# Kernel tuning notes

Hardware: AMD Instinct MI355X
Metric: run time of the kernel (lower is better)

Reference implementation:

```python
import jax, jax.numpy as jnp
import numpy as np
import math

EMBED_DIM = 768
NUM_HEADS = 12


def setup_inputs() -> dict:
    key = jax.random.key(0)
    ks = jax.random.split(key, 5)
    R, C, B, E = 128, 256, 1, EMBED_DIM
    s = 1.0 / math.sqrt(E)
    x = jax.random.normal(ks[0], (R, C, B, E), dtype=jnp.float32)
    wq = jax.random.normal(ks[1], (E, E), dtype=jnp.float32) * s
    wk = jax.random.normal(ks[2], (E, E), dtype=jnp.float32) * s
    wv = jax.random.normal(ks[3], (E, E), dtype=jnp.float32) * s
    wo = jax.random.normal(ks[4], (E, E), dtype=jnp.float32) * s
    z = jnp.zeros((E,), dtype=jnp.float32)
    return {"x": x, "wq": wq, "bq": z, "wk": wk, "bk": z,
            "wv": wv, "bv": z, "wo": wo, "bo": z}


def reference(x, wq, bq, wk, bk, wv, bv, wo, bo):
    R, C, B, E = x.shape
    H = NUM_HEADS
    D = E // H
    shape = (R, C, B, H, D)
    # tied row attention scaling: 1/sqrt(head_dim) * 1/sqrt(num_rows)
    scaling = (D ** -0.5) / math.sqrt(R)
    q = jnp.reshape(x @ wq + bq, shape) * scaling
    k = jnp.reshape(x @ wk + bk, shape)
    v = jnp.reshape(x @ wv + bv, shape)
    # logits summed (tied) over the row axis r: [H, B, C, C]
    attn_weights = jnp.einsum('rinhd,rjnhd->hnij', q, k)
    attn_probs = jax.nn.softmax(attn_weights, axis=-1)
    # broadcast probs back to every row
    context = jnp.einsum('hnij,rjnhd->rinhd', attn_probs, v)
    context = jnp.reshape(context, (R, C, B, E))
    return context @ wo + bo
```

## Files before the change

### kernel.cpp

```cpp
#include <hip/hip_runtime.h>
#include <hip/hip_bf16.h>
#include <math.h>

typedef __bf16 bf16_t;
typedef __bf16 vbf4 __attribute__((ext_vector_type(4)));
typedef __bf16 vbf8 __attribute__((ext_vector_type(8)));
typedef float  vf4  __attribute__((ext_vector_type(4)));

#define OFF_XB   0ull
#define OFF_Q    50331648ull
#define OFF_K    100663296ull
#define OFF_VT   150994944ull
#define OFF_P    201326592ull
#define OFF_WQ   202899456ull
#define OFF_WK   204079104ull
#define OFF_WV   205258752ull
#define OFF_WO   206438400ull

template <int ROWS>
__device__ __forceinline__ void stage_tile(const bf16_t* __restrict__ g,
                                           int ld, int row0, int k0,
                                           bf16_t* lds, int tid) {
  const int wave = tid >> 6;
  const int lane = tid & 63;
  const int js = (lane & 7) ^ (lane >> 3);
#pragma unroll
  for (int cc = 0; cc < ROWS / 32; ++cc) {
    const int chunk = cc * 4 + wave;
    const int row = chunk * 8 + (lane >> 3);
    const bf16_t* gp = g + (size_t)(row0 + row) * ld + k0 + js * 8;
    bf16_t* lp = lds + chunk * 512 + lane * 8;
    __builtin_amdgcn_global_load_lds(
        (const __attribute__((address_space(1))) void*)gp,
        (__attribute__((address_space(3))) void*)lp, 16, 0, 0);
  }
}

__device__ __forceinline__ vbf8 lds_frag(const bf16_t* s, int rr, int ko) {
  const int c = (ko >> 3) ^ (rr & 7);
  return *(const vbf8*)&s[rr * 64 + (c << 3)];
}

__device__ __forceinline__ void gemm_mainloop128(const bf16_t* __restrict__ A, int lda, int m0,
                                                 const bf16_t* __restrict__ Bt, int ldb, int n0,
                                                 int kbeg, int kend,
                                                 bf16_t* As, bf16_t* Bs,
                                                 vf4 (&acc)[4][4]) {
  const int tid = threadIdx.x;
  const int lane = tid & 63;
  const int wave = tid >> 6;
  const int wm0 = (wave >> 1) * 64;
  const int wn0 = (wave & 1) * 64;
  const int fm = lane & 15;
  const int fk = (lane >> 4) * 8;
  for (int k0 = kbeg; k0 < kend; k0 += 64) {
    stage_tile<128>(A, lda, m0, k0, As, tid);
    stage_tile<128>(Bt, ldb, n0, k0, Bs, tid);
    __syncthreads();
#pragma unroll
    for (int kk = 0; kk < 64; kk += 32) {
      vbf8 af[4], bfv[4];
#pragma unroll
      for (int mt = 0; mt < 4; ++mt) af[mt] = lds_frag(As, wm0 + mt * 16 + fm, kk + fk);
#pragma unroll
      for (int nt = 0; nt < 4; ++nt) bfv[nt] = lds_frag(Bs, wn0 + nt * 16 + fm, kk + fk);
#pragma unroll
      for (int mt = 0; mt < 4; ++mt)
#pragma unroll
        for (int nt = 0; nt < 4; ++nt)
          acc[mt][nt] = __builtin_amdgcn_mfma_f32_16x16x32_bf16(af[mt], bfv[nt],
                                                                acc[mt][nt], 0, 0, 0);
    }
    __syncthreads();
  }
}

__device__ __forceinline__ void gemm_mainloop256(const bf16_t* __restrict__ A, int lda, int m0,
                                                 const bf16_t* __restrict__ Bt, int ldb, int n0,
                                                 int kbeg, int kend,
                                                 bf16_t* As, bf16_t* Bs,
                                                 vf4 (&acc)[8][4]) {
  const int tid = threadIdx.x;
  const int lane = tid & 63;
  const int wave = tid >> 6;
  const int wq0 = (wave >> 1) * 64;
  const int wn0 = (wave & 1) * 64;
  const int fm = lane & 15;
  const int fk = (lane >> 4) * 8;
  for (int k0 = kbeg; k0 < kend; k0 += 64) {
    stage_tile<256>(A, lda, m0, k0, As, tid);
    stage_tile<128>(Bt, ldb, n0, k0, Bs, tid);
    __syncthreads();
#pragma unroll
    for (int kk = 0; kk < 64; kk += 32) {
      vbf8 af[8], bfv[4];
#pragma unroll
      for (int mt = 0; mt < 8; ++mt) {
        const int rr = ((mt & 4) << 5) + wq0 + (mt & 3) * 16 + fm;
        af[mt] = lds_frag(As, rr, kk + fk);
      }
#pragma unroll
      for (int nt = 0; nt < 4; ++nt) bfv[nt] = lds_frag(Bs, wn0 + nt * 16 + fm, kk + fk);
#pragma unroll
      for (int mt = 0; mt < 8; ++mt)
#pragma unroll
        for (int nt = 0; nt < 4; ++nt)
          acc[mt][nt] = __builtin_amdgcn_mfma_f32_16x16x32_bf16(af[mt], bfv[nt],
                                                                acc[mt][nt], 0, 0, 0);
    }
    __syncthreads();
  }
}

__device__ __forceinline__ void zero_acc4(vf4 (&acc)[4][4]) {
  const vf4 z = {0.f, 0.f, 0.f, 0.f};
#pragma unroll
  for (int mt = 0; mt < 4; ++mt)
#pragma unroll
    for (int nt = 0; nt < 4; ++nt) acc[mt][nt] = z;
}
__device__ __forceinline__ void zero_acc8(vf4 (&acc)[8][4]) {
  const vf4 z = {0.f, 0.f, 0.f, 0.f};
#pragma unroll
  for (int mt = 0; mt < 8; ++mt)
#pragma unroll
    for (int nt = 0; nt < 4; ++nt) acc[mt][nt] = z;
}

__global__ __launch_bounds__(256) void pack_x(const float* __restrict__ x,
                                              bf16_t* __restrict__ Xb) {
  const size_t idx = (size_t)blockIdx.x * 256 + threadIdx.x;
  const float4 v = ((const float4*)x)[idx];
  vbf4 o;
  o[0] = (bf16_t)v.x; o[1] = (bf16_t)v.y; o[2] = (bf16_t)v.z; o[3] = (bf16_t)v.w;
  ((vbf4*)Xb)[idx] = o;
}

__global__ __launch_bounds__(256) void pack_w(const float* __restrict__ wq,
                                              const float* __restrict__ wk,
                                              const float* __restrict__ wv,
                                              const float* __restrict__ wo,
                                              bf16_t* __restrict__ Wq, bf16_t* __restrict__ Wk,
                                              bf16_t* __restrict__ Wv, bf16_t* __restrict__ Wo,
                                              float scaling) {
  __shared__ float t[64][65];
  const int wid = blockIdx.y;
  const float* src = (wid == 0) ? wq : (wid == 1) ? wk : (wid == 2) ? wv : wo;
  bf16_t* dst = (wid == 0) ? Wq : (wid == 1) ? Wk : (wid == 2) ? Wv : Wo;
  const float sc = (wid == 0) ? scaling : 1.0f;
  const int kt = (blockIdx.x / 12) * 64;
  const int nt = (blockIdx.x % 12) * 64;
  const int tx = threadIdx.x & 63;
  const int ty = threadIdx.x >> 6;
#pragma unroll
  for (int p = 0; p < 16; ++p) {
    const int k = ty + p * 4;
    t[tx][k] = src[(size_t)(kt + k) * 768 + nt + tx] * sc;
  }
  __syncthreads();
#pragma unroll
  for (int p = 0; p < 16; ++p) {
    const int n = ty + p * 4;
    dst[(size_t)(nt + n) * 768 + kt + tx] = (bf16_t)t[n][tx];
  }
}

__global__ __launch_bounds__(256, 2) void qkv_gemm(const bf16_t* __restrict__ Xb,
                                                   const bf16_t* __restrict__ Wq,
                                                   const bf16_t* __restrict__ Wk,
                                                   const bf16_t* __restrict__ Wv,
                                                   const float* __restrict__ bq,
                                                   const float* __restrict__ bk,
                                                   const float* __restrict__ bv,
                                                   bf16_t* __restrict__ Qh,
                                                   bf16_t* __restrict__ Kh,
                                                   bf16_t* __restrict__ Vt,
                                                   float scaling) {
  __shared__ __align__(16) bf16_t As[256 * 64];
  __shared__ __align__(16) bf16_t Bs[128 * 64];
  const int bx = blockIdx.x;
  const int m_idx = bx / 18;
  const int rem = bx - m_idx * 18;
  const int n_idx = rem / 3;
  const int z = rem - n_idx * 3;
  const int m0 = m_idx * 256;
  const int n0 = n_idx * 128;
  const bf16_t* W = (z == 0) ? Wq : (z == 1) ? Wk : Wv;
  vf4 acc[8][4];
  zero_acc8(acc);
  gemm_mainloop256(Xb, 768, m0, W, 768, n0, 0, 768, As, Bs, acc);

  const int lane = threadIdx.x & 63;
  const int wave = threadIdx.x >> 6;
  const int wq0 = (wave >> 1) * 64;
  const int wn0 = (wave & 1) * 64;
  const int col = lane & 15;
  const int rq = (lane >> 4) * 4;
  const float* bias = (z == 0) ? bq : (z == 1) ? bk : bv;
  const float bsc = (z == 0) ? scaling : 1.0f;

  if (z < 2) {
    bf16_t* O = (z == 0) ? Qh : Kh;
#pragma unroll
    for (int mt = 0; mt < 8; ++mt) {
#pragma unroll
      for (int nt = 0; nt < 4; ++nt) {
        const int n = n0 + wn0 + nt * 16 + col;
        const int h = n >> 6, d = n & 63;
        const float bb = bias[n] * bsc;
#pragma unroll
        for (int i = 0; i < 4; ++i) {
          const int m = m0 + ((mt & 4) << 5) + wq0 + (mt & 3) * 16 + rq + i;
          const int r = m >> 8, c = m & 255;
          O[(size_t)(h * 256 + c) * 8192 + (r << 6) + d] = (bf16_t)(acc[mt][nt][i] + bb);
        }
      }
    }
  } else {
#pragma unroll
    for (int mt = 0; mt < 8; ++mt) {
      const int mb = m0 + ((mt & 4) << 5) + wq0 + (mt & 3) * 16 + rq;
      const int r = mb >> 8, c = mb & 255;
#pragma unroll
      for (int nt = 0; nt < 4; ++nt) {
        const int n = n0 + wn0 + nt * 16 + col;
        const int h = n >> 6, d = n & 63;
        const float bb = bias[n];
        vbf4 pk;
#pragma unroll
        for (int i = 0; i < 4; ++i) pk[i] = (bf16_t)(acc[mt][nt][i] + bb);
        *(vbf4*)&Vt[(size_t)h * 2097152 + ((size_t)((r << 6) + d)) * 256 + c] = pk;
      }
    }
  }
}

__global__ __launch_bounds__(256) void logits_gemm(const bf16_t* __restrict__ Qh,
                                                   const bf16_t* __restrict__ Kh,
                                                   float* __restrict__ Lp) {
  __shared__ __align__(16) bf16_t As[128 * 64];
  __shared__ __align__(16) bf16_t Bs[128 * 64];
  const int n0 = blockIdx.x * 128;
  const int m0 = blockIdx.y * 128;
  const int h = blockIdx.z >> 4;
  const int kseg = blockIdx.z & 15;
  const bf16_t* A = Qh + (size_t)h * (256 * 8192);
  const bf16_t* B = Kh + (size_t)h * (256 * 8192);
  vf4 acc[4][4];
  zero_acc4(acc);
  gemm_mainloop128(A, 8192, m0, B, 8192, n0, kseg * 512, kseg * 512 + 512, As, Bs, acc);

  const int lane = threadIdx.x & 63;
  const int wave = threadIdx.x >> 6;
  const int wm0 = (wave >> 1) * 64;
  const int wn0 = (wave & 1) * 64;
  const int col = lane & 15;
  const int rq = (lane >> 4) * 4;
  float* Lph = Lp + ((size_t)(kseg * 12 + h)) * 65536;
#pragma unroll
  for (int mt = 0; mt < 4; ++mt)
#pragma unroll
    for (int nt = 0; nt < 4; ++nt) {
      const int n = n0 + wn0 + nt * 16 + col;
#pragma unroll
      for (int i = 0; i < 4; ++i) {
        const int m = m0 + wm0 + mt * 16 + rq + i;
        Lph[(size_t)m * 256 + n] = acc[mt][nt][i];
      }
    }
}

__global__ __launch_bounds__(256) void softmax_k(const float* __restrict__ Lp,
                                                 bf16_t* __restrict__ P) {
  const int row = blockIdx.x * 4 + (threadIdx.x >> 6);
  const int lane = threadIdx.x & 63;
  float a = 0.f, b = 0.f, c = 0.f, d = 0.f;
#pragma unroll
  for (int ks = 0; ks < 16; ++ks) {
    const float4 v4 = ((const float4*)(Lp + (size_t)ks * 786432 + (size_t)row * 256))[lane];
    a += v4.x; b += v4.y; c += v4.z; d += v4.w;
  }
  float mx = fmaxf(fmaxf(a, b), fmaxf(c, d));
#pragma unroll
  for (int off = 32; off; off >>= 1) mx = fmaxf(mx, __shfl_xor(mx, off));
  a = expf(a - mx); b = expf(b - mx); c = expf(c - mx); d = expf(d - mx);
  float s = a + b + c + d;
#pragma unroll
  for (int off = 32; off; off >>= 1) s += __shfl_xor(s, off);
  const float inv = 1.0f / s;
  vbf4 o;
  o[0] = (bf16_t)(a * inv); o[1] = (bf16_t)(b * inv);
  o[2] = (bf16_t)(c * inv); o[3] = (bf16_t)(d * inv);
  ((vbf4*)(P + (size_t)row * 256))[lane] = o;
}

__global__ __launch_bounds__(256, 2) void ctx_gemm(const bf16_t* __restrict__ P,
                                                   const bf16_t* __restrict__ Vt,
                                                   bf16_t* __restrict__ CtxTok) {
  __shared__ __align__(16) bf16_t As[256 * 64];
  __shared__ __align__(16) bf16_t Bs[128 * 64];
  const int n0 = blockIdx.x * 128;
  const int h = blockIdx.y;
  const bf16_t* A = P + (size_t)h * 65536;
  const bf16_t* B = Vt + (size_t)h * 2097152;
  vf4 acc[8][4];
  zero_acc8(acc);
  gemm_mainloop256(A, 256, 0, B, 256, n0, 0, 256, As, Bs, acc);

  const int lane = threadIdx.x & 63;
  const int wave = threadIdx.x >> 6;
  const int wq0 = (wave >> 1) * 64;
  const int wn0 = (wave & 1) * 64;
  const int col = lane & 15;
  const int rq = (lane >> 4) * 4;
#pragma unroll
  for (int mt = 0; mt < 8; ++mt)
#pragma unroll
    for (int nt = 0; nt < 4; ++nt) {
      const int n = n0 + wn0 + nt * 16 + col;
      const int r = n >> 6, d = n & 63;
#pragma unroll
      for (int i = 0; i < 4; ++i) {
        const int m = ((mt & 4) << 5) + wq0 + (mt & 3) * 16 + rq + i;
        CtxTok[(size_t)((r << 8) + m) * 768 + (h << 6) + d] = (bf16_t)acc[mt][nt][i];
      }
    }
}

__global__ __launch_bounds__(256, 2) void out_gemm(const bf16_t* __restrict__ Ctx,
                                                   const bf16_t* __restrict__ Wo,
                                                   const float* __restrict__ bo,
                                                   float* __restrict__ Out) {
  __shared__ __align__(16) bf16_t As[256 * 64];
  __shared__ __align__(16) bf16_t Bs[128 * 64];
  const int bx = blockIdx.x;
  const int m_idx = bx / 6;
  const int n_idx = bx - m_idx * 6;
  const int m0 = m_idx * 256;
  const int n0 = n_idx * 128;
  vf4 acc[8][4];
  zero_acc8(acc);
  gemm_mainloop256(Ctx, 768, m0, Wo, 768, n0, 0, 768, As, Bs, acc);

  const int lane = threadIdx.x & 63;
  const int wave = threadIdx.x >> 6;
  const int wq0 = (wave >> 1) * 64;
  const int wn0 = (wave & 1) * 64;
  const int col = lane & 15;
  const int rq = (lane >> 4) * 4;
#pragma unroll
  for (int mt = 0; mt < 8; ++mt)
#pragma unroll
    for (int nt = 0; nt < 4; ++nt) {
      const int n = n0 + wn0 + nt * 16 + col;
      const float bb = bo[n];
#pragma unroll
      for (int i = 0; i < 4; ++i) {
        const int m = m0 + ((mt & 4) << 5) + wq0 + (mt & 3) * 16 + rq + i;
        Out[(size_t)m * 768 + n] = acc[mt][nt][i] + bb;
      }
    }
}

extern "C" void kernel_launch(void* const* d_in, const int* in_sizes, int n_in,
                              void* d_out, int out_size, void* d_ws, size_t ws_size,
                              hipStream_t stream) {
  const float* x  = (const float*)d_in[0];
  const float* wq = (const float*)d_in[1];
  const float* bq = (const float*)d_in[2];
  const float* wk = (const float*)d_in[3];
  const float* bk = (const float*)d_in[4];
  const float* wv = (const float*)d_in[5];
  const float* bv = (const float*)d_in[6];
  const float* wo = (const float*)d_in[7];
  const float* bo = (const float*)d_in[8];
  float* out = (float*)d_out;

  char* ws = (char*)d_ws;
  bf16_t* Xb  = (bf16_t*)(ws + OFF_XB);
  float*  Lp  = (float*)(ws + OFF_XB);
  bf16_t* Ctx = (bf16_t*)(ws + OFF_XB);
  bf16_t* Qh  = (bf16_t*)(ws + OFF_Q);
  bf16_t* Kh  = (bf16_t*)(ws + OFF_K);
  bf16_t* Vt  = (bf16_t*)(ws + OFF_VT);
  bf16_t* P   = (bf16_t*)(ws + OFF_P);
  bf16_t* Wq  = (bf16_t*)(ws + OFF_WQ);
  bf16_t* Wk  = (bf16_t*)(ws + OFF_WK);
  bf16_t* Wv  = (bf16_t*)(ws + OFF_WV);
  bf16_t* Wo  = (bf16_t*)(ws + OFF_WO);

  const float scaling = 0.125f / sqrtf(128.0f);

  pack_x<<<24576, 256, 0, stream>>>(x, Xb);
  pack_w<<<dim3(144, 4), 256, 0, stream>>>(wq, wk, wv, wo, Wq, Wk, Wv, Wo, scaling);
  qkv_gemm<<<2304, 256, 0, stream>>>(Xb, Wq, Wk, Wv, bq, bk, bv, Qh, Kh, Vt, scaling);
  logits_gemm<<<dim3(2, 2, 192), 256, 0, stream>>>(Qh, Kh, Lp);
  softmax_k<<<768, 256, 0, stream>>>(Lp, P);
  ctx_gemm<<<dim3(64, 12), 256, 0, stream>>>(P, Vt, Ctx);
  out_gemm<<<768, 256, 0, stream>>>(Ctx, Wo, bo, out);

  (void)in_sizes; (void)n_in; (void)out_size; (void)ws_size;
}
```

Measured before the change: 454.6 us.

## Double-buffer 256x256 GEMM tiles with 8-wave interleaved async staging

Replaces the single-buffered 256x128 GEMM mainloop with a double-buffered 256x256 pipeline run by 512-thread blocks. Global-to-LDS loads for the next K step are issued in quarters between MFMA phases, synchronised with explicit vmcnt waits, raw barriers and setprio. This applies to the QKV, context and output projection GEMMs and halves their grid sizes. The aim is to hide load latency and reuse each tile across more outputs. In exchange the block uses 128KB of LDS, which limits occupancy, and correctness depends on the hand-placed waitcnt and barrier ordering.

```diff
diff --git a/kernel.cpp b/kernel.cpp
--- a/kernel.cpp
+++ b/kernel.cpp
@@ -27,6 +27,24 @@
 #pragma unroll
   for (int cc = 0; cc < ROWS / 32; ++cc) {
     const int chunk = cc * 4 + wave;
+    const int row = chunk * 8 + (lane >> 3);
+    const bf16_t* gp = g + (size_t)(row0 + row) * ld + k0 + js * 8;
+    bf16_t* lp = lds + chunk * 512 + lane * 8;
+    __builtin_amdgcn_global_load_lds(
+        (const __attribute__((address_space(1))) void*)gp,
+        (__attribute__((address_space(3))) void*)lp, 16, 0, 0);
+  }
+}
+
+__device__ __forceinline__ void stage_half(const bf16_t* __restrict__ g,
+                                           int ld, int row0, int k0,
+                                           bf16_t* lds, int half, int tid) {
+  const int wave = tid >> 6;
+  const int lane = tid & 63;
+  const int js = (lane & 7) ^ (lane >> 3);
+#pragma unroll
+  for (int cc = 0; cc < 2; ++cc) {
+    const int chunk = half * 16 + cc * 8 + wave;
     const int row = chunk * 8 + (lane >> 3);
     const bf16_t* gp = g + (size_t)(row0 + row) * ld + k0 + js * 8;
     bf16_t* lp = lds + chunk * 512 + lane * 8;
@@ -75,40 +93,76 @@
   }
 }
 
-__device__ __forceinline__ void gemm_mainloop256(const bf16_t* __restrict__ A, int lda, int m0,
-                                                 const bf16_t* __restrict__ Bt, int ldb, int n0,
-                                                 int kbeg, int kend,
-                                                 bf16_t* As, bf16_t* Bs,
-                                                 vf4 (&acc)[8][4]) {
+__device__ __forceinline__ void gemm_pipe256(const bf16_t* __restrict__ A, int lda, int m0,
+                                             const bf16_t* __restrict__ Bt, int ldb, int n0,
+                                             int nt,
+                                             bf16_t (&As)[2][256 * 64],
+                                             bf16_t (&Bs)[2][256 * 64],
+                                             vf4 (&acc)[8][4]) {
   const int tid = threadIdx.x;
   const int lane = tid & 63;
   const int wave = tid >> 6;
-  const int wq0 = (wave >> 1) * 64;
-  const int wn0 = (wave & 1) * 64;
+  const int aRow0 = (wave >> 2) * 128;
+  const int bRow0 = (wave & 3) * 64;
   const int fm = lane & 15;
   const int fk = (lane >> 4) * 8;
-  for (int k0 = kbeg; k0 < kend; k0 += 64) {
-    stage_tile<256>(A, lda, m0, k0, As, tid);
-    stage_tile<128>(Bt, ldb, n0, k0, Bs, tid);
-    __syncthreads();
-#pragma unroll
-    for (int kk = 0; kk < 64; kk += 32) {
-      vbf8 af[8], bfv[4];
-#pragma unroll
-      for (int mt = 0; mt < 8; ++mt) {
-        const int rr = ((mt & 4) << 5) + wq0 + (mt & 3) * 16 + fm;
-        af[mt] = lds_frag(As, rr, kk + fk);
-      }
-#pragma unroll
-      for (int nt = 0; nt < 4; ++nt) bfv[nt] = lds_frag(Bs, wn0 + nt * 16 + fm, kk + fk);
-#pragma unroll
-      for (int mt = 0; mt < 8; ++mt)
-#pragma unroll
-        for (int nt = 0; nt < 4; ++nt)
-          acc[mt][nt] = __builtin_amdgcn_mfma_f32_16x16x32_bf16(af[mt], bfv[nt],
-                                                                acc[mt][nt], 0, 0, 0);
-    }
-    __syncthreads();
+
+  stage_half(A, lda, m0, 0, As[0], 0, tid);
+  stage_half(A, lda, m0, 0, As[0], 1, tid);
+  stage_half(Bt, ldb, n0, 0, Bs[0], 0, tid);
+  stage_half(Bt, ldb, n0, 0, Bs[0], 1, tid);
+  if (nt > 1) {
+    stage_half(Bt, ldb, n0, 64, Bs[1], 0, tid);
+    stage_half(Bt, ldb, n0, 64, Bs[1], 1, tid);
+    asm volatile("s_waitcnt vmcnt(4)" ::: "memory");
+  } else {
+    asm volatile("s_waitcnt vmcnt(0)" ::: "memory");
+  }
+  __builtin_amdgcn_s_barrier();
+
+  for (int t = 0; t < nt; ++t) {
+    const int cur = t & 1;
+    bf16_t* as = As[cur];
+    bf16_t* bs = Bs[cur];
+    bf16_t* an = As[cur ^ 1];
+    vbf8 bfv[4][2];
+#pragma unroll
+    for (int q = 0; q < 4; ++q) {
+      vbf8 af[2][2];
+#pragma unroll
+      for (int m2 = 0; m2 < 2; ++m2)
+#pragma unroll
+        for (int kk = 0; kk < 2; ++kk)
+          af[m2][kk] = lds_frag(as, aRow0 + q * 32 + m2 * 16 + fm, kk * 32 + fk);
+      if (q == 0) {
+#pragma unroll
+        for (int bn = 0; bn < 4; ++bn)
+#pragma unroll
+          for (int kk = 0; kk < 2; ++kk)
+            bfv[bn][kk] = lds_frag(bs, bRow0 + bn * 16 + fm, kk * 32 + fk);
+      }
+      if (q < 2) {
+        if (t + 1 < nt) stage_half(A, lda, m0, (t + 1) * 64, an, q, tid);
+      } else {
+        if (t + 2 < nt) stage_half(Bt, ldb, n0, (t + 2) * 64, bs, q - 2, tid);
+      }
+      __builtin_amdgcn_s_barrier();
+      __builtin_amdgcn_s_setprio(1);
+#pragma unroll
+      for (int m2 = 0; m2 < 2; ++m2)
+#pragma unroll
+        for (int bn = 0; bn < 4; ++bn)
+#pragma unroll
+          for (int kk = 0; kk < 2; ++kk)
+            acc[q * 2 + m2][bn] = __builtin_amdgcn_mfma_f32_16x16x32_bf16(
+                af[m2][kk], bfv[bn][kk], acc[q * 2 + m2][bn], 0, 0, 0);
+      __builtin_amdgcn_s_setprio(0);
+      if (q < 3) __builtin_amdgcn_s_barrier();
+    }
+    const int rem = nt - 1 - t;
+    if (rem >= 2)      asm volatile("s_waitcnt vmcnt(4)" ::: "memory");
+    else if (rem == 1) asm volatile("s_waitcnt vmcnt(0)" ::: "memory");
+    __builtin_amdgcn_s_barrier();
   }
 }
 
@@ -165,7 +219,7 @@
   }
 }
 
-__global__ __launch_bounds__(256, 2) void qkv_gemm(const bf16_t* __restrict__ Xb,
+__global__ __launch_bounds__(512, 2) void qkv_gemm(const bf16_t* __restrict__ Xb,
                                                    const bf16_t* __restrict__ Wq,
                                                    const bf16_t* __restrict__ Wk,
                                                    const bf16_t* __restrict__ Wv,
@@ -176,24 +230,24 @@
                                                    bf16_t* __restrict__ Kh,
                                                    bf16_t* __restrict__ Vt,
                                                    float scaling) {
-  __shared__ __align__(16) bf16_t As[256 * 64];
-  __shared__ __align__(16) bf16_t Bs[128 * 64];
+  __shared__ __align__(16) bf16_t As[2][256 * 64];
+  __shared__ __align__(16) bf16_t Bs[2][256 * 64];
   const int bx = blockIdx.x;
-  const int m_idx = bx / 18;
-  const int rem = bx - m_idx * 18;
+  const int m_idx = bx / 9;
+  const int rem = bx - m_idx * 9;
   const int n_idx = rem / 3;
   const int z = rem - n_idx * 3;
   const int m0 = m_idx * 256;
-  const int n0 = n_idx * 128;
+  const int n0 = n_idx * 256;
   const bf16_t* W = (z == 0) ? Wq : (z == 1) ? Wk : Wv;
   vf4 acc[8][4];
   zero_acc8(acc);
-  gemm_mainloop256(Xb, 768, m0, W, 768, n0, 0, 768, As, Bs, acc);
+  gemm_pipe256(Xb, 768, m0, W, 768, n0, 12, As, Bs, acc);
 
   const int lane = threadIdx.x & 63;
   const int wave = threadIdx.x >> 6;
-  const int wq0 = (wave >> 1) * 64;
-  const int wn0 = (wave & 1) * 64;
+  const int aRow0 = (wave >> 2) * 128;
+  const int bRow0 = (wave & 3) * 64;
   const int col = lane & 15;
   const int rq = (lane >> 4) * 4;
   const float* bias = (z == 0) ? bq : (z == 1) ? bk : bv;
@@ -205,12 +259,12 @@
     for (int mt = 0; mt < 8; ++mt) {
 #pragma unroll
       for (int nt = 0; nt < 4; ++nt) {
-        const int n = n0 + wn0 + nt * 16 + col;
+        const int n = n0 + bRow0 + nt * 16 + col;
         const int h = n >> 6, d = n & 63;
         const float bb = bias[n] * bsc;
 #pragma unroll
         for (int i = 0; i < 4; ++i) {
-          const int m = m0 + ((mt & 4) << 5) + wq0 + (mt & 3) * 16 + rq + i;
+          const int m = m0 + aRow0 + mt * 16 + rq + i;
           const int r = m >> 8, c = m & 255;
           O[(size_t)(h * 256 + c) * 8192 + (r << 6) + d] = (bf16_t)(acc[mt][nt][i] + bb);
         }
@@ -219,11 +273,11 @@
   } else {
 #pragma unroll
     for (int mt = 0; mt < 8; ++mt) {
-      const int mb = m0 + ((mt & 4) << 5) + wq0 + (mt & 3) * 16 + rq;
+      const int mb = m0 + aRow0 + mt * 16 + rq;
       const int r = mb >> 8, c = mb & 255;
 #pragma unroll
       for (int nt = 0; nt < 4; ++nt) {
-        const int n = n0 + wn0 + nt * 16 + col;
+        const int n = n0 + bRow0 + nt * 16 + col;
         const int h = n >> 6, d = n & 63;
         const float bb = bias[n];
         vbf4 pk;
@@ -294,69 +348,69 @@
   ((vbf4*)(P + (size_t)row * 256))[lane] = o;
 }
 
-__global__ __launch_bounds__(256, 2) void ctx_gemm(const bf16_t* __restrict__ P,
+__global__ __launch_bounds__(512, 2) void ctx_gemm(const bf16_t* __restrict__ P,
                                                    const bf16_t* __restrict__ Vt,
                                                    bf16_t* __restrict__ CtxTok) {
-  __shared__ __align__(16) bf16_t As[256 * 64];
-  __shared__ __align__(16) bf16_t Bs[128 * 64];
-  const int n0 = blockIdx.x * 128;
+  __shared__ __align__(16) bf16_t As[2][256 * 64];
+  __shared__ __align__(16) bf16_t Bs[2][256 * 64];
+  const int n0 = blockIdx.x * 256;
   const int h = blockIdx.y;
   const bf16_t* A = P + (size_t)h * 65536;
   const bf16_t* B = Vt + (size_t)h * 2097152;
   vf4 acc[8][4];
   zero_acc8(acc);
-  gemm_mainloop256(A, 256, 0, B, 256, n0, 0, 256, As, Bs, acc);
+  gemm_pipe256(A, 256, 0, B, 256, n0, 4, As, Bs, acc);
 
   const int lane = threadIdx.x & 63;
   const int wave = threadIdx.x >> 6;
-  const int wq0 = (wave >> 1) * 64;
-  const int wn0 = (wave & 1) * 64;
+  const int aRow0 = (wave >> 2) * 128;
+  const int bRow0 = (wave & 3) * 64;
   const int col = lane & 15;
   const int rq = (lane >> 4) * 4;
 #pragma unroll
   for (int mt = 0; mt < 8; ++mt)
 #pragma unroll
     for (int nt = 0; nt < 4; ++nt) {
-      const int n = n0 + wn0 + nt * 16 + col;
+      const int n = n0 + bRow0 + nt * 16 + col;
       const int r = n >> 6, d = n & 63;
 #pragma unroll
       for (int i = 0; i < 4; ++i) {
-        const int m = ((mt & 4) << 5) + wq0 + (mt & 3) * 16 + rq + i;
+        const int m = aRow0 + mt * 16 + rq + i;
         CtxTok[(size_t)((r << 8) + m) * 768 + (h << 6) + d] = (bf16_t)acc[mt][nt][i];
       }
     }
 }
 
-__global__ __launch_bounds__(256, 2) void out_gemm(const bf16_t* __restrict__ Ctx,
+__global__ __launch_bounds__(512, 2) void out_gemm(const bf16_t* __restrict__ Ctx,
                                                    const bf16_t* __restrict__ Wo,
                                                    const float* __restrict__ bo,
                                                    float* __restrict__ Out) {
-  __shared__ __align__(16) bf16_t As[256 * 64];
-  __shared__ __align__(16) bf16_t Bs[128 * 64];
+  __shared__ __align__(16) bf16_t As[2][256 * 64];
+  __shared__ __align__(16) bf16_t Bs[2][256 * 64];
   const int bx = blockIdx.x;
-  const int m_idx = bx / 6;
-  const int n_idx = bx - m_idx * 6;
+  const int m_idx = bx / 3;
+  const int n_idx = bx - m_idx * 3;
   const int m0 = m_idx * 256;
-  const int n0 = n_idx * 128;
+  const int n0 = n_idx * 256;
   vf4 acc[8][4];
   zero_acc8(acc);
-  gemm_mainloop256(Ctx, 768, m0, Wo, 768, n0, 0, 768, As, Bs, acc);
+  gemm_pipe256(Ctx, 768, m0, Wo, 768, n0, 12, As, Bs, acc);
 
   const int lane = threadIdx.x & 63;
   const int wave = threadIdx.x >> 6;
-  const int wq0 = (wave >> 1) * 64;
-  const int wn0 = (wave & 1) * 64;
+  const int aRow0 = (wave >> 2) * 128;
+  const int bRow0 = (wave & 3) * 64;
   const int col = lane & 15;
   const int rq = (lane >> 4) * 4;
 #pragma unroll
   for (int mt = 0; mt < 8; ++mt)
 #pragma unroll
     for (int nt = 0; nt < 4; ++nt) {
-      const int n = n0 + wn0 + nt * 16 + col;
+      const int n = n0 + bRow0 + nt * 16 + col;
       const float bb = bo[n];
 #pragma unroll
       for (int i = 0; i < 4; ++i) {
-        const int m = m0 + ((mt & 4) << 5) + wq0 + (mt & 3) * 16 + rq + i;
+        const int m = m0 + aRow0 + mt * 16 + rq + i;
         Out[(size_t)m * 768 + n] = acc[mt][nt][i] + bb;
       }
     }
@@ -393,11 +447,11 @@
 
   pack_x<<<24576, 256, 0, stream>>>(x, Xb);
   pack_w<<<dim3(144, 4), 256, 0, stream>>>(wq, wk, wv, wo, Wq, Wk, Wv, Wo, scaling);
-  qkv_gemm<<<2304, 256, 0, stream>>>(Xb, Wq, Wk, Wv, bq, bk, bv, Qh, Kh, Vt, scaling);
+  qkv_gemm<<<1152, 512, 0, stream>>>(Xb, Wq, Wk, Wv, bq, bk, bv, Qh, Kh, Vt, scaling);
   logits_gemm<<<dim3(2, 2, 192), 256, 0, stream>>>(Qh, Kh, Lp);
   softmax_k<<<768, 256, 0, stream>>>(Lp, P);
-  ctx_gemm<<<dim3(64, 12), 256, 0, stream>>>(P, Vt, Ctx);
-  out_gemm<<<768, 256, 0, stream>>>(Ctx, Wo, bo, out);
+  ctx_gemm<<<dim3(32, 12), 512, 0, stream>>>(P, Vt, Ctx);
+  out_gemm<<<384, 512, 0, stream>>>(Ctx, Wo, bo, out);
 
   (void)in_sizes; (void)n_in; (void)out_size; (void)ws_size;
 }
```

Measured after the change: 483.7 us. +6.4%, slower.
